# Kernel tuning notes

Measured on AMD Instinct MI355X. Metric: run time of the kernel, lower is better.

## Reference

```python
import jax, jax.numpy as jnp
import numpy as np

B, DIN, H, DOUT = 8192, 1024, 2048, 1024
P, E = 4, 6            # n_patches, n_edges
C = H // P             # per-patch feature dim = 512
IDX_I = jnp.array([0, 0, 0, 1, 1, 2])  # i<j pair order matches nested loop
IDX_J = jnp.array([1, 2, 3, 2, 3, 3])


def setup_inputs() -> dict:
    key = jax.random.key(0)
    ks = jax.random.split(key, 12)
    s = 0.02
    return {
        "x": jax.random.normal(ks[0], (B, DIN), jnp.float32),
        "fiber": jax.random.normal(ks[1], (B, C), jnp.float32),  # randn_like(base) in torch fwd
        "W_in": jax.random.normal(ks[2], (DIN, H), jnp.float32) * s,
        "b_in": jnp.zeros((H,), jnp.float32),
        "incidence": jax.random.normal(ks[3], (E, P), jnp.float32) * 0.1,
        "sheaf_maps": jnp.tile((jnp.eye(C, dtype=jnp.float32) * 0.1)[None], (E, 1, 1)),
        "damping": jnp.float32(0.1),
        "Wb": jax.random.normal(ks[4], (P, C, C // 2), jnp.float32) * s,
        "bb": jnp.zeros((P, C // 2), jnp.float32),
        "Wf": jax.random.normal(ks[5], (P, C, C // 2), jnp.float32) * s,
        "bf": jnp.zeros((P, C // 2), jnp.float32),
        "Wt": jax.random.normal(ks[6], (C, C), jnp.float32) * s,
        "bt": jnp.zeros((C,), jnp.float32),
        "Wr": jax.random.normal(ks[7], (E, C, C // 2), jnp.float32) * s,
        "br": jnp.zeros((E, C // 2), jnp.float32),
        "Wg": jax.random.normal(ks[8], (H, H), jnp.float32) * s,
        "bg": jnp.zeros((H,), jnp.float32),
        "Wc": jax.random.normal(ks[9], (H + C, DOUT), jnp.float32) * s,
        "bc": jnp.zeros((DOUT,), jnp.float32),
    }


def reference(x, fiber, W_in, b_in, incidence, sheaf_maps, damping,
              Wb, bb, Wf, bf, Wt, bt, Wr, br, Wg, bg, Wc, bc):
    # input projection + split into P contiguous chunks (stack == reshape)
    h = x @ W_in + b_in                                      # [B, H]
    sections = h.reshape(B, P, C)                            # [B, P, C]

    # --- NeuralSheafLaplacian ---
    # coboundary: incidence-weighted combination of patch sections, then per-edge sheaf map
    weighted = jnp.einsum('ep,bpc->bec', incidence, sections)          # [B, E, C]
    coboundary = jnp.einsum('bec,ecd->bed', weighted, sheaf_maps)      # [B, E, C]
    L = incidence.T @ incidence                                        # [P, P] = delta^T delta
    diffused = sections - damping * jnp.einsum('pq,bqc->bpc', L, sections)
    h1_norm = jnp.linalg.norm(coboundary, axis=-1).mean(axis=-1)       # [B]

    # --- FiberBundleLayer ---
    base = diffused.mean(axis=1)                                       # [B, C]
    b_proj = jnp.einsum('bc,scd->bsd', base, Wb) + bb                  # [B, P, C/2]
    f_proj = jnp.einsum('bc,scd->bsd', fiber, Wf) + bf                 # [B, P, C/2]
    simplices = jnp.concatenate([b_proj, f_proj], axis=-1) @ Wt + bt   # [B, P, C]
    total = simplices.mean(axis=1)                                     # [B, C]

    # --- CohomologyConsistency ---
    si = diffused[:, IDX_I]                                            # [B, E, C]
    sj = diffused[:, IDX_J]                                            # [B, E, C]
    ri = jnp.einsum('bec,ecd->bed', si, Wr) + br
    rj = jnp.einsum('bec,ecd->bed', sj, Wr) + br
    h1_loss = jnp.mean((ri - rj) ** 2, axis=(0, 2)).mean()             # mean of per-pair MSEs
    glued = diffused.reshape(B, H) @ Wg + bg                           # cat(sections) == reshape

    output = jnp.concatenate([glued, total], axis=-1) @ Wc + bc        # [B, DOUT]
    return output, diffused, h1_norm, h1_loss, total
```

## Files before the change

kernel.cpp:

```cpp
#include <hip/hip_runtime.h>
#include <cstdint>

#define B_    8192
#define DIN_  1024
#define H_    2048
#define DOUT_ 1024
#define P4_   4
#define E6_   6
#define C_    512
#define C2_   256

typedef __bf16 bf16x8 __attribute__((ext_vector_type(8)));
typedef float  f32x4  __attribute__((ext_vector_type(4)));

__device__ __forceinline__ unsigned short f2bf_bits(float f) {
    unsigned u = __float_as_uint(f);
    unsigned r = (u + 0x7fffu + ((u >> 16) & 1u)) >> 16;
    return (unsigned short)r;
}
__device__ __forceinline__ float bf2f(unsigned short s) {
    return __uint_as_float(((unsigned)s) << 16);
}

__device__ __forceinline__ void async_load16(void* lds, const void* g) {
    __builtin_amdgcn_global_load_lds(
        (__attribute__((address_space(1))) void*)(uintptr_t)g,
        (__attribute__((address_space(3))) void*)(unsigned int)(uintptr_t)lds,
        16, 0, 0);
}


__global__ void convert_f32_bf16_k(const float* __restrict__ in,
                                   unsigned short* __restrict__ out, int n) {
    int i = (blockIdx.x * blockDim.x + threadIdx.x) * 4;
    if (i + 3 < n) {
        float4 v = *(const float4*)(in + i);
        ushort4 o;
        o.x = f2bf_bits(v.x); o.y = f2bf_bits(v.y);
        o.z = f2bf_bits(v.z); o.w = f2bf_bits(v.w);
        *(ushort4*)(out + i) = o;
    }
}

__global__ void transpose_to_bf16_k(const float* __restrict__ in,
                                    unsigned short* __restrict__ out,
                                    int R, int Cc, long inStrideZ, long outStrideZ) {
    __shared__ float t[32][33];
    in  += (long)blockIdx.z * inStrideZ;
    out += (long)blockIdx.z * outStrideZ;
    int x0 = blockIdx.x << 5, y0 = blockIdx.y << 5;
    int tx = threadIdx.x, ty = threadIdx.y;
#pragma unroll
    for (int j = 0; j < 32; j += 8)
        t[ty + j][tx] = in[(long)(y0 + ty + j) * Cc + x0 + tx];
    __syncthreads();
#pragma unroll
    for (int j = 0; j < 32; j += 8)
        out[(long)(x0 + ty + j) * R + y0 + tx] = f2bf_bits(t[tx][ty + j]);
}

__global__ void wbar_k(const float* __restrict__ W, unsigned short* __restrict__ outT) {
    int id = blockIdx.x * blockDim.x + threadIdx.x;
    int d = id >> 9, c = id & 511;
    float s = 0.f;
#pragma unroll
    for (int si = 0; si < 4; si++) s += W[si * (512 * 256) + c * 256 + d];
    outT[id] = f2bf_bits(0.25f * s);
}

__global__ void bbar_k(const float* __restrict__ b, float* __restrict__ out) {
    int d = threadIdx.x;
    out[d] = 0.25f * (b[d] + b[256 + d] + b[512 + d] + b[768 + d]);
}

__global__ void copy_wc_tail_k(const unsigned short* __restrict__ src,
                               unsigned short* __restrict__ dst) {
    int id = blockIdx.x * 256 + threadIdx.x;
    int n = id >> 7, c4 = (id & 127) << 2;
    long off = (long)n * 2560 + 2048 + c4;
    *(ushort4*)(dst + off) = *(const ushort4*)(src + off);
}

__global__ void bout_k(const float* __restrict__ bg, const float* __restrict__ Wc,
                       const float* __restrict__ bc, float* __restrict__ bout) {
    int n = blockIdx.x * 256 + threadIdx.x;
    int j0 = blockIdx.y << 7;
    float s = (blockIdx.y == 0) ? bc[n] : 0.f;
#pragma unroll 4
    for (int j = 0; j < 128; j++) s += bg[j0 + j] * Wc[(long)(j0 + j) * 1024 + n];
    atomicAdd(&bout[n], s);
}

__global__ void k2_diffuse_k(const unsigned short* __restrict__ hb,
                             const float* __restrict__ incidence,
                             const float* __restrict__ damping,
                             float* __restrict__ outDiff,
                             unsigned short* __restrict__ diffb,
                             unsigned short* __restrict__ baseb,
                             unsigned short* __restrict__ weightedb,
                             unsigned short* __restrict__ debuf) {
    __shared__ float M4[4][4];
    __shared__ float inc2[24];
    int tid = threadIdx.x;
    if (tid < 16) {
        int p = tid >> 2, q = tid & 3;
        float l = 0.f;
#pragma unroll
        for (int e = 0; e < 6; e++) l += incidence[e * 4 + p] * incidence[e * 4 + q];
        M4[p][q] = (p == q ? 1.f : 0.f) - damping[0] * l;
    }
    if (tid < 24) inc2[tid] = incidence[tid];
    __syncthreads();

    int b = blockIdx.x >> 1;
    int c = ((blockIdx.x & 1) << 8) + tid;
    long hoff = (long)b * H_ + c;
    long doff = (long)b * 2560 + c;
    float s0 = bf2f(hb[hoff]);
    float s1 = bf2f(hb[hoff + 512]);
    float s2 = bf2f(hb[hoff + 1024]);
    float s3 = bf2f(hb[hoff + 1536]);

    float d0 = M4[0][0]*s0 + M4[0][1]*s1 + M4[0][2]*s2 + M4[0][3]*s3;
    float d1 = M4[1][0]*s0 + M4[1][1]*s1 + M4[1][2]*s2 + M4[1][3]*s3;
    float d2 = M4[2][0]*s0 + M4[2][1]*s1 + M4[2][2]*s2 + M4[2][3]*s3;
    float d3 = M4[3][0]*s0 + M4[3][1]*s1 + M4[3][2]*s2 + M4[3][3]*s3;

    outDiff[hoff]        = d0;
    outDiff[hoff + 512]  = d1;
    outDiff[hoff + 1024] = d2;
    outDiff[hoff + 1536] = d3;
    diffb[doff]        = f2bf_bits(d0);
    diffb[doff + 512]  = f2bf_bits(d1);
    diffb[doff + 1024] = f2bf_bits(d2);
    diffb[doff + 1536] = f2bf_bits(d3);
    baseb[(long)b * C_ + c] = f2bf_bits(0.25f * (d0 + d1 + d2 + d3));

#pragma unroll
    for (int e = 0; e < 6; e++) {
        float w = inc2[e*4+0]*s0 + inc2[e*4+1]*s1 + inc2[e*4+2]*s2 + inc2[e*4+3]*s3;
        weightedb[(long)e * (B_ * (long)C_) + (long)b * C_ + c] = f2bf_bits(w);
    }
    float dI[6] = {d0, d0, d0, d1, d1, d2};
    float dJ[6] = {d1, d2, d3, d2, d3, d3};
#pragma unroll
    for (int e = 0; e < 6; e++)
        debuf[(long)e * (B_ * (long)C_) + (long)b * C_ + c] = f2bf_bits(dI[e] - dJ[e]);
}

template <int MODE>
__global__ __launch_bounds__(256, 2)
void gemm_bt_k(const unsigned short* __restrict__ A, long sAz, int lda,
               const unsigned short* __restrict__ Bt, long sBz, int K,
               const float* __restrict__ bias,
               unsigned short* __restrict__ Cb, int ldcb,
               float* __restrict__ Cf, int ldcf,
               float* __restrict__ red, long sRz) {
    __shared__ __align__(16) unsigned short smA[128 * 64];
    __shared__ __align__(16) unsigned short smB[128 * 64];
    const int tid = threadIdx.x;
    const int lane = tid & 63, w = tid >> 6;
    const int wm = w >> 1, wn = w & 1;
    const int m16 = lane & 15, quad = lane >> 4;
    const int m7 = m16 & 7;

    const int nwg = gridDim.x * gridDim.y;
    const int bid = blockIdx.y * gridDim.x + blockIdx.x;
    const int lid = (nwg & 7) ? bid : (((bid & 7) * (nwg >> 3)) + (bid >> 3));
    const int bx = lid % gridDim.x;
    const int by = lid / gridDim.x;

    A  += (long)blockIdx.z * sAz;
    Bt += (long)blockIdx.z * sBz;
    const long rowA0 = (long)by * 128;
    const long rowB0 = (long)bx * 128;

    f32x4 acc[4][4];
#pragma unroll
    for (int i = 0; i < 4; i++)
#pragma unroll
        for (int j = 0; j < 4; j++) acc[i][j] = f32x4{0.f, 0.f, 0.f, 0.f};

    for (int k0 = 0; k0 < K; k0 += 64) {
#pragma unroll
        for (int i = 0; i < 4; i++) {
            int chunk = i * 256 + tid;
            int row = chunk >> 3;
            int keS = ((chunk & 7) ^ (row & 7)) << 3;
            async_load16(&smA[chunk << 3], A  + (rowA0 + row) * (long)lda + k0 + keS);
            async_load16(&smB[chunk << 3], Bt + (rowB0 + row) * (long)K   + k0 + keS);
        }
        __syncthreads();
#pragma unroll
        for (int kk = 0; kk < 64; kk += 32) {
            const int pc = (((kk >> 3) + quad) ^ m7) << 3;
            bf16x8 af[4], bfv[4];
#pragma unroll
            for (int i = 0; i < 4; i++) {
                af[i]  = *(const bf16x8*)&smA[((wm << 6) + (i << 4) + m16) * 64 + pc];
                bfv[i] = *(const bf16x8*)&smB[((wn << 6) + (i << 4) + m16) * 64 + pc];
            }
#pragma unroll
            for (int i = 0; i < 4; i++)
#pragma unroll
                for (int j = 0; j < 4; j++)
                    acc[i][j] = __builtin_amdgcn_mfma_f32_16x16x32_bf16(af[i], bfv[j], acc[i][j], 0, 0, 0);
        }
        __syncthreads();
    }

    const long rowBase = rowA0 + (wm << 6);
    const long colBase = rowB0 + (wn << 6);

    if (MODE <= 2) {
#pragma unroll
        for (int j = 0; j < 4; j++) {
            long col = colBase + (j << 4) + m16;
            float bv = bias ? bias[col] : 0.f;
#pragma unroll
            for (int i = 0; i < 4; i++) {
                long row = rowBase + (i << 4) + (quad << 2);
#pragma unroll
                for (int r = 0; r < 4; r++) {
                    float v = acc[i][j][r] + bv;
                    if (MODE == 0 || MODE == 2) Cb[(row + r) * (long)ldcb + col] = f2bf_bits(v);
                    if (MODE == 1 || MODE == 2) Cf[(row + r) * (long)ldcf + col] = v;
                }
            }
        }
    } else if (MODE == 3) {
        float* rz = red + (long)blockIdx.z * sRz;
#pragma unroll
        for (int i = 0; i < 4; i++) {
            float v0 = 0.f, v1 = 0.f, v2 = 0.f, v3 = 0.f;
#pragma unroll
            for (int j = 0; j < 4; j++) {
                float a0 = acc[i][j][0], a1 = acc[i][j][1], a2 = acc[i][j][2], a3 = acc[i][j][3];
                v0 += a0 * a0; v1 += a1 * a1; v2 += a2 * a2; v3 += a3 * a3;
            }
#pragma unroll
            for (int m = 1; m <= 8; m <<= 1) {
                v0 += __shfl_xor(v0, m); v1 += __shfl_xor(v1, m);
                v2 += __shfl_xor(v2, m); v3 += __shfl_xor(v3, m);
            }
            if (m16 == 0) {
                long row = rowBase + (i << 4) + (quad << 2);
                atomicAdd(&rz[row + 0], v0);
                atomicAdd(&rz[row + 1], v1);
                atomicAdd(&rz[row + 2], v2);
                atomicAdd(&rz[row + 3], v3);
            }
        }
    } else {
        float s = 0.f;
#pragma unroll
        for (int i = 0; i < 4; i++)
#pragma unroll
            for (int j = 0; j < 4; j++)
#pragma unroll
                for (int r = 0; r < 4; r++) { float a = acc[i][j][r]; s += a * a; }
#pragma unroll
        for (int m = 1; m <= 32; m <<= 1) s += __shfl_xor(s, m);
        if (lane == 0) atomicAdd(red, s);
    }
}

__global__ void f1_h1norm_k(const float* __restrict__ hn, float* __restrict__ out) {
    int b = blockIdx.x * 256 + threadIdx.x;
    float s = 0.f;
#pragma unroll
    for (int e = 0; e < 6; e++) s += sqrtf(hn[e * B_ + b]);
    out[b] = s * (1.f / 6.f);
}

__global__ void f2_h1loss_k(const float* __restrict__ acc, float* __restrict__ out) {
    if (threadIdx.x == 0) out[0] = acc[0] * (1.f / (8192.f * 6.f * 256.f));
}

extern "C" void kernel_launch(void* const* d_in, const int* in_sizes, int n_in,
                              void* d_out, int out_size, void* d_ws, size_t ws_size,
                              hipStream_t stream) {
    const float* x     = (const float*)d_in[0];
    const float* fiber = (const float*)d_in[1];
    const float* W_in  = (const float*)d_in[2];
    const float* b_in  = (const float*)d_in[3];
    const float* incid = (const float*)d_in[4];
    const float* sheaf = (const float*)d_in[5];
    const float* damp  = (const float*)d_in[6];
    const float* Wb    = (const float*)d_in[7];
    const float* bb    = (const float*)d_in[8];
    const float* Wf    = (const float*)d_in[9];
    const float* bfv   = (const float*)d_in[10];
    const float* Wt    = (const float*)d_in[11];
    const float* bt    = (const float*)d_in[12];
    const float* Wr    = (const float*)d_in[13];
    const float* Wg    = (const float*)d_in[15];
    const float* bg    = (const float*)d_in[16];
    const float* Wc    = (const float*)d_in[17];
    const float* bc    = (const float*)d_in[18];

    float* out      = (float*)d_out;
    float* outDiff  = out + 8388608;
    float* outH1n   = out + 25165824;
    float* outH1l   = out + 25174016;
    float* outTotal = out + 25174017;

    char* ws = (char*)d_ws;
    size_t o = 0;
    auto alloc = [&](size_t bytes) { size_t r = o; o += (bytes + 255) & ~(size_t)255; return r; };

    size_t r0 = alloc(50331648);
    unsigned short* xb = (unsigned short*)(ws + r0);
    unsigned short* hb = (unsigned short*)(ws + r0 + 16777216);
    unsigned short* Ab2560    = (unsigned short*)(ws + alloc(41943040));
    unsigned short* baseb     = (unsigned short*)(ws + alloc(8388608));
    unsigned short* weightedb = (unsigned short*)(ws + alloc(50331648));
    unsigned short* debuf     = (unsigned short*)(ws + alloc(50331648));
    unsigned short* fiberb    = (unsigned short*)(ws + alloc(8388608));
    unsigned short* cbar      = (unsigned short*)(ws + alloc(8388608));
    unsigned short* WinT   = (unsigned short*)(ws + alloc(4194304));
    unsigned short* Wgb    = (unsigned short*)(ws + alloc(8388608));
    unsigned short* WcT    = (unsigned short*)(ws + alloc(5242880));
    unsigned short* WoutT  = (unsigned short*)(ws + alloc(5242880));
    unsigned short* WtT    = (unsigned short*)(ws + alloc(524288));
    unsigned short* WrT    = (unsigned short*)(ws + alloc(1572864));
    unsigned short* ShT    = (unsigned short*)(ws + alloc(3145728));
    unsigned short* WbBarT = (unsigned short*)(ws + alloc(262144));
    unsigned short* WfBarT = (unsigned short*)(ws + alloc(262144));
    float* bbarf  = (float*)(ws + alloc(1024));
    float* bfbarf = (float*)(ws + alloc(1024));
    float* boutf  = (float*)(ws + alloc(4096));
    float* hnacc  = (float*)(ws + alloc(6 * 8192 * 4 + 256));
    float* lossacc = hnacc + 6 * 8192;

    (void)hipMemsetAsync(hnacc, 0, 6 * 8192 * 4 + 256, stream);
    (void)hipMemsetAsync(boutf, 0, 4096, stream);

    convert_f32_bf16_k<<<8192, 256, 0, stream>>>(x, xb, 8388608);
    convert_f32_bf16_k<<<4096, 256, 0, stream>>>(fiber, fiberb, 4194304);
    convert_f32_bf16_k<<<4096, 256, 0, stream>>>(Wg, Wgb, 4194304);
    dim3 tb(32, 8);
    transpose_to_bf16_k<<<dim3(64, 32), tb, 0, stream>>>(W_in, WinT, 1024, 2048, 0, 0);
    transpose_to_bf16_k<<<dim3(32, 80), tb, 0, stream>>>(Wc, WcT, 2560, 1024, 0, 0);
    transpose_to_bf16_k<<<dim3(16, 16), tb, 0, stream>>>(Wt, WtT, 512, 512, 0, 0);
    transpose_to_bf16_k<<<dim3(16, 16, 6), tb, 0, stream>>>(sheaf, ShT, 512, 512, 512 * 512, 512 * 512);
    transpose_to_bf16_k<<<dim3(8, 16, 6), tb, 0, stream>>>(Wr, WrT, 512, 256, 512 * 256, 512 * 256);
    wbar_k<<<512, 256, 0, stream>>>(Wb, WbBarT);
    wbar_k<<<512, 256, 0, stream>>>(Wf, WfBarT);
    bbar_k<<<1, 256, 0, stream>>>(bb, bbarf);
    bbar_k<<<1, 256, 0, stream>>>(bfv, bfbarf);

    gemm_bt_k<0><<<dim3(16, 8, 1), 256, 0, stream>>>(WcT, 0, 2560, Wgb, 0, H_,
                                                     nullptr, WoutT, 2560, nullptr, 0, nullptr, 0);
    copy_wc_tail_k<<<512, 256, 0, stream>>>(WcT, WoutT);
    bout_k<<<dim3(4, 16), 256, 0, stream>>>(bg, Wc, bc, boutf);

    gemm_bt_k<0><<<dim3(16, 64, 1), 256, 0, stream>>>(xb, 0, DIN_, WinT, 0, DIN_,
                                                      b_in, hb, H_, nullptr, 0, nullptr, 0);
    k2_diffuse_k<<<16384, 256, 0, stream>>>(hb, incid, damp, outDiff, Ab2560, baseb, weightedb, debuf);

    gemm_bt_k<3><<<dim3(4, 64, 6), 256, 0, stream>>>(weightedb, (long)B_ * C_, C_, ShT, (long)C_ * C_, C_,
                                                     nullptr, nullptr, 0, nullptr, 0, hnacc, B_);
    gemm_bt_k<4><<<dim3(2, 64, 6), 256, 0, stream>>>(debuf, (long)B_ * C_, C_, WrT, (long)C2_ * C_, C_,
                                                     nullptr, nullptr, 0, nullptr, 0, lossacc, 0);
    gemm_bt_k<0><<<dim3(2, 64, 1), 256, 0, stream>>>(baseb, 0, C_, WbBarT, 0, C_,
                                                     bbarf, cbar, C_, nullptr, 0, nullptr, 0);
    gemm_bt_k<0><<<dim3(2, 64, 1), 256, 0, stream>>>(fiberb, 0, C_, WfBarT, 0, C_,
                                                     bfbarf, cbar + 256, C_, nullptr, 0, nullptr, 0);
    gemm_bt_k<2><<<dim3(4, 64, 1), 256, 0, stream>>>(cbar, 0, C_, WtT, 0, C_,
                                                     bt, Ab2560 + 2048, 2560, outTotal, C_, nullptr, 0);
    gemm_bt_k<1><<<dim3(8, 64, 1), 256, 0, stream>>>(Ab2560, 0, 2560, WoutT, 0, 2560,
                                                     boutf, nullptr, 0, out, DOUT_, nullptr, 0);
    f1_h1norm_k<<<32, 256, 0, stream>>>(hnacc, outH1n);
    f2_h1loss_k<<<1, 64, 0, stream>>>(lossacc, outH1l);

    (void)in_sizes; (void)n_in; (void)out_size; (void)ws_size;
}
```

Measured before the change: 586.0 us.

## Fold fiber-bundle projections into Wt and split-K weight precompute

Precomputes a combined weight WcombT = [WbBar; WfBar] composed with Wt, plus a folded bias, so the fiber-bundle path becomes one K=1024 GEMM over concatenated [base, fiber] activations instead of three GEMMs with an intermediate cbar buffer. The Wc·Wg weight-product GEMM is also split along K across two z-slices that accumulate into an fp32 buffer through atomics, then get converted to bf16, which adds parallelism to a small-grid launch. The cost is extra small kernels, a memset, fp32 atomics and slightly different rounding from pre-multiplying the weights.

```diff
diff --git a/kernel.cpp b/kernel.cpp
--- a/kernel.cpp
+++ b/kernel.cpp
@@ -42,6 +42,17 @@
     }
 }
 
+__global__ void convert_fiber_k(const float* __restrict__ in,
+                                unsigned short* __restrict__ out) {
+    int idx4 = (blockIdx.x * 256 + threadIdx.x) * 4;
+    int b = idx4 >> 9, c = idx4 & 511;
+    float4 v = *(const float4*)(in + idx4);
+    ushort4 o;
+    o.x = f2bf_bits(v.x); o.y = f2bf_bits(v.y);
+    o.z = f2bf_bits(v.z); o.w = f2bf_bits(v.w);
+    *(ushort4*)(out + (long)b * 1024 + 512 + c) = o;
+}
+
 __global__ void transpose_to_bf16_k(const float* __restrict__ in,
                                     unsigned short* __restrict__ out,
                                     int R, int Cc, long inStrideZ, long outStrideZ) {
@@ -59,18 +70,28 @@
         out[(long)(x0 + ty + j) * R + y0 + tx] = f2bf_bits(t[tx][ty + j]);
 }
 
-__global__ void wbar_k(const float* __restrict__ W, unsigned short* __restrict__ outT) {
+__global__ void wbar_k(const float* __restrict__ W, unsigned short* __restrict__ out) {
     int id = blockIdx.x * blockDim.x + threadIdx.x;
-    int d = id >> 9, c = id & 511;
     float s = 0.f;
 #pragma unroll
-    for (int si = 0; si < 4; si++) s += W[si * (512 * 256) + c * 256 + d];
-    outT[id] = f2bf_bits(0.25f * s);
+    for (int si = 0; si < 4; si++) s += W[si * (512 * 256) + id];
+    out[id] = f2bf_bits(0.25f * s);
 }
 
 __global__ void bbar_k(const float* __restrict__ b, float* __restrict__ out) {
     int d = threadIdx.x;
     out[d] = 0.25f * (b[d] + b[256 + d] + b[512 + d] + b[768 + d]);
+}
+
+__global__ void btot_k(const float* __restrict__ bbar, const float* __restrict__ bfbar,
+                       const float* __restrict__ Wt, const float* __restrict__ bt,
+                       float* __restrict__ btot) {
+    int n = blockIdx.x * 256 + threadIdx.x;
+    float s = bt[n];
+#pragma unroll 4
+    for (int d = 0; d < 256; d++)
+        s += bbar[d] * Wt[d * 512 + n] + bfbar[d] * Wt[(256 + d) * 512 + n];
+    btot[n] = s;
 }
 
 __global__ void copy_wc_tail_k(const unsigned short* __restrict__ src,
@@ -79,6 +100,16 @@
     int n = id >> 7, c4 = (id & 127) << 2;
     long off = (long)n * 2560 + 2048 + c4;
     *(ushort4*)(dst + off) = *(const ushort4*)(src + off);
+}
+
+__global__ void wout_conv_k(const float* __restrict__ in, unsigned short* __restrict__ out) {
+    int idx4 = (blockIdx.x * 256 + threadIdx.x) * 4;
+    int n = idx4 >> 11, k = idx4 & 2047;
+    float4 v = *(const float4*)(in + idx4);
+    ushort4 o;
+    o.x = f2bf_bits(v.x); o.y = f2bf_bits(v.y);
+    o.z = f2bf_bits(v.z); o.w = f2bf_bits(v.w);
+    *(ushort4*)(out + (long)n * 2560 + k) = o;
 }
 
 __global__ void bout_k(const float* __restrict__ bg, const float* __restrict__ Wc,
@@ -96,7 +127,7 @@
                              const float* __restrict__ damping,
                              float* __restrict__ outDiff,
                              unsigned short* __restrict__ diffb,
-                             unsigned short* __restrict__ baseb,
+                             unsigned short* __restrict__ basefib,
                              unsigned short* __restrict__ weightedb,
                              unsigned short* __restrict__ debuf) {
     __shared__ float M4[4][4];
@@ -134,7 +165,7 @@
     diffb[doff + 512]  = f2bf_bits(d1);
     diffb[doff + 1024] = f2bf_bits(d2);
     diffb[doff + 1536] = f2bf_bits(d3);
-    baseb[(long)b * C_ + c] = f2bf_bits(0.25f * (d0 + d1 + d2 + d3));
+    basefib[(long)b * 1024 + c] = f2bf_bits(0.25f * (d0 + d1 + d2 + d3));
 
 #pragma unroll
     for (int e = 0; e < 6; e++) {
@@ -151,10 +182,10 @@
 template <int MODE>
 __global__ __launch_bounds__(256, 2)
 void gemm_bt_k(const unsigned short* __restrict__ A, long sAz, int lda,
-               const unsigned short* __restrict__ Bt, long sBz, int K,
+               const unsigned short* __restrict__ Bt, long sBz, int ldb, int K,
                const float* __restrict__ bias,
                unsigned short* __restrict__ Cb, int ldcb,
-               float* __restrict__ Cf, int ldcf,
+               float* __restrict__ Cf, int ldcf, long sCz,
                float* __restrict__ red, long sRz) {
     __shared__ __align__(16) unsigned short smA[128 * 64];
     __shared__ __align__(16) unsigned short smB[128 * 64];
@@ -188,7 +219,7 @@
             int row = chunk >> 3;
             int keS = ((chunk & 7) ^ (row & 7)) << 3;
             async_load16(&smA[chunk << 3], A  + (rowA0 + row) * (long)lda + k0 + keS);
-            async_load16(&smB[chunk << 3], Bt + (rowB0 + row) * (long)K   + k0 + keS);
+            async_load16(&smB[chunk << 3], Bt + (rowB0 + row) * (long)ldb + k0 + keS);
         }
         __syncthreads();
 #pragma unroll
@@ -213,6 +244,8 @@
     const long colBase = rowB0 + (wn << 6);
 
     if (MODE <= 2) {
+        Cb += (long)blockIdx.z * sCz;
+        Cf += (long)blockIdx.z * sCz;
 #pragma unroll
         for (int j = 0; j < 4; j++) {
             long col = colBase + (j << 4) + m16;
@@ -251,7 +284,7 @@
                 atomicAdd(&rz[row + 3], v3);
             }
         }
-    } else {
+    } else if (MODE == 4) {
         float s = 0.f;
 #pragma unroll
         for (int i = 0; i < 4; i++)
@@ -262,6 +295,18 @@
 #pragma unroll
         for (int m = 1; m <= 32; m <<= 1) s += __shfl_xor(s, m);
         if (lane == 0) atomicAdd(red, s);
+    } else {
+#pragma unroll
+        for (int j = 0; j < 4; j++) {
+            long col = colBase + (j << 4) + m16;
+#pragma unroll
+            for (int i = 0; i < 4; i++) {
+                long row = rowBase + (i << 4) + (quad << 2);
+#pragma unroll
+                for (int r = 0; r < 4; r++)
+                    atomicAdd(&Cf[(row + r) * (long)ldcf + col], acc[i][j][r]);
+            }
+        }
     }
 }
 
@@ -313,31 +358,32 @@
     unsigned short* xb = (unsigned short*)(ws + r0);
     unsigned short* hb = (unsigned short*)(ws + r0 + 16777216);
     unsigned short* Ab2560    = (unsigned short*)(ws + alloc(41943040));
-    unsigned short* baseb     = (unsigned short*)(ws + alloc(8388608));
+    unsigned short* basefibb  = (unsigned short*)(ws + alloc(16777216));
     unsigned short* weightedb = (unsigned short*)(ws + alloc(50331648));
     unsigned short* debuf     = (unsigned short*)(ws + alloc(50331648));
-    unsigned short* fiberb    = (unsigned short*)(ws + alloc(8388608));
-    unsigned short* cbar      = (unsigned short*)(ws + alloc(8388608));
     unsigned short* WinT   = (unsigned short*)(ws + alloc(4194304));
     unsigned short* Wgb    = (unsigned short*)(ws + alloc(8388608));
     unsigned short* WcT    = (unsigned short*)(ws + alloc(5242880));
     unsigned short* WoutT  = (unsigned short*)(ws + alloc(5242880));
+    float*          WoutF  = (float*)(ws + alloc(8388608));
     unsigned short* WtT    = (unsigned short*)(ws + alloc(524288));
     unsigned short* WrT    = (unsigned short*)(ws + alloc(1572864));
     unsigned short* ShT    = (unsigned short*)(ws + alloc(3145728));
-    unsigned short* WbBarT = (unsigned short*)(ws + alloc(262144));
-    unsigned short* WfBarT = (unsigned short*)(ws + alloc(262144));
+    unsigned short* WbarCat= (unsigned short*)(ws + alloc(524288));
+    unsigned short* WcombT = (unsigned short*)(ws + alloc(1048576));
     float* bbarf  = (float*)(ws + alloc(1024));
     float* bfbarf = (float*)(ws + alloc(1024));
+    float* btotf  = (float*)(ws + alloc(2048));
     float* boutf  = (float*)(ws + alloc(4096));
     float* hnacc  = (float*)(ws + alloc(6 * 8192 * 4 + 256));
     float* lossacc = hnacc + 6 * 8192;
 
     (void)hipMemsetAsync(hnacc, 0, 6 * 8192 * 4 + 256, stream);
     (void)hipMemsetAsync(boutf, 0, 4096, stream);
+    (void)hipMemsetAsync(WoutF, 0, 8388608, stream);
 
     convert_f32_bf16_k<<<8192, 256, 0, stream>>>(x, xb, 8388608);
-    convert_f32_bf16_k<<<4096, 256, 0, stream>>>(fiber, fiberb, 4194304);
+    convert_fiber_k<<<4096, 256, 0, stream>>>(fiber, basefibb);
     convert_f32_bf16_k<<<4096, 256, 0, stream>>>(Wg, Wgb, 4194304);
     dim3 tb(32, 8);
     transpose_to_bf16_k<<<dim3(64, 32), tb, 0, stream>>>(W_in, WinT, 1024, 2048, 0, 0);
@@ -345,32 +391,32 @@
     transpose_to_bf16_k<<<dim3(16, 16), tb, 0, stream>>>(Wt, WtT, 512, 512, 0, 0);
     transpose_to_bf16_k<<<dim3(16, 16, 6), tb, 0, stream>>>(sheaf, ShT, 512, 512, 512 * 512, 512 * 512);
     transpose_to_bf16_k<<<dim3(8, 16, 6), tb, 0, stream>>>(Wr, WrT, 512, 256, 512 * 256, 512 * 256);
-    wbar_k<<<512, 256, 0, stream>>>(Wb, WbBarT);
-    wbar_k<<<512, 256, 0, stream>>>(Wf, WfBarT);
+    wbar_k<<<512, 256, 0, stream>>>(Wb, WbarCat);
+    wbar_k<<<512, 256, 0, stream>>>(Wf, WbarCat + 131072);
     bbar_k<<<1, 256, 0, stream>>>(bb, bbarf);
     bbar_k<<<1, 256, 0, stream>>>(bfv, bfbarf);
-
-    gemm_bt_k<0><<<dim3(16, 8, 1), 256, 0, stream>>>(WcT, 0, 2560, Wgb, 0, H_,
-                                                     nullptr, WoutT, 2560, nullptr, 0, nullptr, 0);
+    btot_k<<<2, 256, 0, stream>>>(bbarf, bfbarf, Wt, bt, btotf);
+
+    gemm_bt_k<0><<<dim3(4, 4, 2), 256, 0, stream>>>(WtT, 256, 512, WbarCat, 131072, 256, 256,
+                                                    nullptr, WcombT, 1024, nullptr, 0, 512, nullptr, 0);
+    gemm_bt_k<5><<<dim3(16, 8, 2), 256, 0, stream>>>(WcT, 1024, 2560, Wgb, 1024, 2048, 1024,
+                                                     nullptr, nullptr, 0, WoutF, 2048, 0, nullptr, 0);
+    wout_conv_k<<<2048, 256, 0, stream>>>(WoutF, WoutT);
     copy_wc_tail_k<<<512, 256, 0, stream>>>(WcT, WoutT);
     bout_k<<<dim3(4, 16), 256, 0, stream>>>(bg, Wc, bc, boutf);
 
-    gemm_bt_k<0><<<dim3(16, 64, 1), 256, 0, stream>>>(xb, 0, DIN_, WinT, 0, DIN_,
-                                                      b_in, hb, H_, nullptr, 0, nullptr, 0);
-    k2_diffuse_k<<<16384, 256, 0, stream>>>(hb, incid, damp, outDiff, Ab2560, baseb, weightedb, debuf);
-
-    gemm_bt_k<3><<<dim3(4, 64, 6), 256, 0, stream>>>(weightedb, (long)B_ * C_, C_, ShT, (long)C_ * C_, C_,
-                                                     nullptr, nullptr, 0, nullptr, 0, hnacc, B_);
-    gemm_bt_k<4><<<dim3(2, 64, 6), 256, 0, stream>>>(debuf, (long)B_ * C_, C_, WrT, (long)C2_ * C_, C_,
-                                                     nullptr, nullptr, 0, nullptr, 0, lossacc, 0);
-    gemm_bt_k<0><<<dim3(2, 64, 1), 256, 0, stream>>>(baseb, 0, C_, WbBarT, 0, C_,
-                                                     bbarf, cbar, C_, nullptr, 0, nullptr, 0);
-    gemm_bt_k<0><<<dim3(2, 64, 1), 256, 0, stream>>>(fiberb, 0, C_, WfBarT, 0, C_,
-                                                     bfbarf, cbar + 256, C_, nullptr, 0, nullptr, 0);
-    gemm_bt_k<2><<<dim3(4, 64, 1), 256, 0, stream>>>(cbar, 0, C_, WtT, 0, C_,
-                                                     bt, Ab2560 + 2048, 2560, outTotal, C_, nullptr, 0);
-    gemm_bt_k<1><<<dim3(8, 64, 1), 256, 0, stream>>>(Ab2560, 0, 2560, WoutT, 0, 2560,
-                                                     boutf, nullptr, 0, out, DOUT_, nullptr, 0);
+    gemm_bt_k<0><<<dim3(16, 64, 1), 256, 0, stream>>>(xb, 0, DIN_, WinT, 0, DIN_, DIN_,
+                                                      b_in, hb, H_, nullptr, 0, 0, nullptr, 0);
+    k2_diffuse_k<<<16384, 256, 0, stream>>>(hb, incid, damp, outDiff, Ab2560, basefibb, weightedb, debuf);
+
+    gemm_bt_k<3><<<dim3(4, 64, 6), 256, 0, stream>>>(weightedb, (long)B_ * C_, C_, ShT, (long)C_ * C_, C_, C_,
+                                                     nullptr, nullptr, 0, nullptr, 0, 0, hnacc, B_);
+    gemm_bt_k<4><<<dim3(2, 64, 6), 256, 0, stream>>>(debuf, (long)B_ * C_, C_, WrT, (long)C2_ * C_, C_, C_,
+                                                     nullptr, nullptr, 0, nullptr, 0, 0, lossacc, 0);
+    gemm_bt_k<2><<<dim3(4, 64, 1), 256, 0, stream>>>(basefibb, 0, 1024, WcombT, 0, 1024, 1024,
+                                                     btotf, Ab2560 + 2048, 2560, outTotal, C_, 0, nullptr, 0);
+    gemm_bt_k<1><<<dim3(8, 64, 1), 256, 0, stream>>>(Ab2560, 0, 2560, WoutT, 0, 2560, 2560,
+                                                     boutf, nullptr, 0, out, DOUT_, 0, nullptr, 0);
     f1_h1norm_k<<<32, 256, 0, stream>>>(hnacc, outH1n);
     f2_h1loss_k<<<1, 64, 0, stream>>>(lossacc, outH1l);
 
```

New measurement: 605.5 us. +3.3%, slower.
